# Performance work log

Hardware: AMD Instinct MI355X
Metric: run time of the kernel (lower is better)

Reference implementation:

```python
import jax, jax.numpy as jnp
import numpy as np

N = 50000
E = 800000
D = 64
EPS_BN = 1e-5
EPS_NORM = 1e-12


def _bn_train(x, gamma, beta):
    # BatchNorm1d in training mode: batch stats over axis 0, biased variance
    mu = jnp.mean(x, axis=0, keepdims=True)
    var = jnp.mean((x - mu) ** 2, axis=0, keepdims=True)
    return (x - mu) / jnp.sqrt(var + EPS_BN) * gamma + beta


def setup_inputs() -> dict:
    key = jax.random.key(0)
    ks = jax.random.split(key, 16)
    s = 1.0 / np.sqrt(D)
    s2 = 1.0 / np.sqrt(2 * D)
    return {
        "h": jax.random.normal(ks[0], (N, D), jnp.float32),
        "e": jax.random.normal(ks[1], (E, D), jnp.float32),
        "src": jax.random.randint(ks[2], (E,), 0, N, jnp.int32),
        "dst": jax.random.randint(ks[3], (E,), 0, N, jnp.int32),
        "A_W": jax.random.uniform(ks[4], (D, D), jnp.float32, -s, s),
        "A_b": jax.random.uniform(ks[5], (D,), jnp.float32, -s, s),
        "B_W": jax.random.uniform(ks[6], (D, D), jnp.float32, -s, s),
        "B_b": jax.random.uniform(ks[7], (D,), jnp.float32, -s, s),
        "C_W": jax.random.uniform(ks[8], (D, D), jnp.float32, -s, s),
        "C_b": jax.random.uniform(ks[9], (D,), jnp.float32, -s, s),
        "W_apply": jax.random.uniform(ks[10], (2 * D, D), jnp.float32, -s2, s2),
        "b_apply": jax.random.uniform(ks[11], (D,), jnp.float32, -s2, s2),
        "gamma_h": jnp.ones((D,), jnp.float32),
        "beta_h": jnp.zeros((D,), jnp.float32),
        "gamma_e": jnp.ones((D,), jnp.float32),
        "beta_e": jnp.zeros((D,), jnp.float32),
    }


def reference(h, e, src, dst, A_W, A_b, B_W, B_b, C_W, C_b,
              W_apply, b_apply, gamma_h, beta_h, gamma_e, beta_e):
    h_in, e_in = h, e
    # dropout p=0 -> identity
    Ah = h @ A_W + A_b            # [N, D]
    Bh = h @ B_W + B_b            # [N, D]
    Ce = e @ C_W + C_b            # [E, D]

    # message: e_ij = Ce + Bh_src + Bh_dst ; gated message sigma(e_ij)*Ah_src
    e_ij = Ce + Bh[src] + Bh[dst]                 # [E, D]
    msg = jax.nn.relu(jax.nn.sigmoid(e_ij) * Ah[src])  # [E, D]

    # reduce: per-destination-node max over mailbox
    c = jax.ops.segment_max(msg, dst, num_segments=N)  # [N, D], -inf if empty
    deg = jax.ops.segment_sum(jnp.ones((E,), msg.dtype), dst, num_segments=N)
    c = jnp.where(deg[:, None] > 0, c, 0.0)

    # apply/update: concat -> linear -> L2 normalize -> activation
    bundle = jnp.concatenate([h, c], axis=1) @ W_apply + b_apply  # [N, D]
    norm = jnp.sqrt(jnp.sum(bundle * bundle, axis=1, keepdims=True))
    bundle = bundle / jnp.maximum(norm, EPS_NORM)
    h_new = jax.nn.relu(bundle)

    e_new = jax.nn.relu(e_ij)

    h_new = _bn_train(h_new, gamma_h, beta_h)
    e_new = _bn_train(e_new, gamma_e, beta_e)

    h_out = h_in + h_new
    e_out = e_in + e_new
    return (h_out, e_out)
```

## Files before the change

kernel.cpp:

```cpp
#include <hip/hip_runtime.h>

typedef __attribute__((ext_vector_type(8))) short short8;
typedef __attribute__((ext_vector_type(4))) float f32x4;
typedef __attribute__((ext_vector_type(4))) unsigned int u32x4;

#define DEV static __device__ __forceinline__

constexpr int NN = 50000;
constexpr int NE = 800000;
constexpr int NT_N = NN / 16;
constexpr int NT_E = NE / 16;
constexpr int NB_SCAN = (NN + 255) / 256;
constexpr float EPS_BN = 1e-5f;
constexpr float EPS_NORM = 1e-12f;

DEV unsigned short f2b(float f) {
  unsigned u = __float_as_uint(f);
  return (unsigned short)((u + 0x7FFFu + ((u >> 16) & 1u)) >> 16);
}

DEV short8 load_a_frag(const float* __restrict__ base, int row, int kbase) {
  const f32x4* p = reinterpret_cast<const f32x4*>(base + row * 64 + kbase);
  f32x4 v0 = p[0], v1 = p[1];
  short8 a;
  a[0] = f2b(v0[0]); a[1] = f2b(v0[1]); a[2] = f2b(v0[2]); a[3] = f2b(v0[3]);
  a[4] = f2b(v1[0]); a[5] = f2b(v1[1]); a[6] = f2b(v1[2]); a[7] = f2b(v1[3]);
  return a;
}

DEV short8 load_w_frag(const float* __restrict__ W, int kbase, int c0, int lane) {
  int kr = kbase + ((lane >> 4) << 3);
  int cc = c0 + (lane & 15);
  short8 b;
#pragma unroll
  for (int j = 0; j < 8; ++j) b[j] = f2b(W[(kr + j) * 64 + cc]);
  return b;
}

DEV f32x4 mfma16(short8 a, short8 b, f32x4 c) {
  return __builtin_amdgcn_mfma_f32_16x16x32_bf16(a, b, c, 0, 0, 0);
}

__global__ void k_init(u32x4* __restrict__ cbuf4, int* __restrict__ deg,
                       float* __restrict__ stats) {
  int i = blockIdx.x * 256 + threadIdx.x;
  u32x4 z = {0u, 0u, 0u, 0u};
  cbuf4[i] = z;
  if (i < NN) deg[i] = 0;
  if (i < 512) stats[i] = 0.0f;
}

__global__ void k_deg(const int* __restrict__ dst, int* __restrict__ deg) {
  int i = blockIdx.x * 256 + threadIdx.x;
  if (i < NE) atomicAdd(&deg[dst[i]], 1);
}

__global__ void k_scan_local(const int* __restrict__ deg, int* __restrict__ off,
                             int* __restrict__ bsum) {
  __shared__ int sh[256];
  int t = threadIdx.x;
  int i = blockIdx.x * 256 + t;
  int v = (i < NN) ? deg[i] : 0;
  sh[t] = v;
  __syncthreads();
  for (int s = 1; s < 256; s <<= 1) {
    int u = (t >= s) ? sh[t - s] : 0;
    __syncthreads();
    sh[t] += u;
    __syncthreads();
  }
  if (i < NN) off[i] = sh[t] - v;
  if (t == 255) bsum[blockIdx.x] = sh[255];
}

__global__ void k_scan_base(const int* __restrict__ bsum, int* __restrict__ bbase) {
  __shared__ int sh[256];
  int t = threadIdx.x;
  int v = (t < NB_SCAN) ? bsum[t] : 0;
  sh[t] = v;
  __syncthreads();
  for (int s = 1; s < 256; s <<= 1) {
    int u = (t >= s) ? sh[t - s] : 0;
    __syncthreads();
    sh[t] += u;
    __syncthreads();
  }
  if (t < NB_SCAN) bbase[t] = sh[t] - v;
}

__global__ void k_scan_fix(const int* __restrict__ bbase, int* __restrict__ off,
                           int* __restrict__ cursor) {
  int i = blockIdx.x * 256 + threadIdx.x;
  if (i < NN) {
    int o = off[i] + bbase[blockIdx.x];
    off[i] = o;
    cursor[i] = o;
  }
}

__global__ void k_scatter(const int* __restrict__ dst, int* __restrict__ cursor,
                          int* __restrict__ perm) {
  int i = blockIdx.x * 256 + threadIdx.x;
  if (i < NE) {
    int p = atomicAdd(&cursor[dst[i]], 1);
    perm[p] = i;
  }
}

__global__ void __launch_bounds__(256) k_node_lin(
    const float* __restrict__ h, const float* __restrict__ AW,
    const float* __restrict__ Ab, const float* __restrict__ BW,
    const float* __restrict__ Bb, float* __restrict__ Ah_p,
    float* __restrict__ Bh_p) {
  int lane = threadIdx.x & 63, warp = threadIdx.x >> 6;
  int tile = blockIdx.x * 4 + warp;
  if (tile >= NT_N) return;
  int r = lane & 15;

  short8 wa[4][2], wb[4][2];
  float ab[4], bb[4];
#pragma unroll
  for (int t = 0; t < 4; ++t) {
#pragma unroll
    for (int kk = 0; kk < 2; ++kk) {
      wa[t][kk] = load_w_frag(AW, kk * 32, t * 16, lane);
      wb[t][kk] = load_w_frag(BW, kk * 32, t * 16, lane);
    }
    ab[t] = Ab[t * 16 + r];
    bb[t] = Bb[t * 16 + r];
  }

  int row0 = tile * 16;
  int ar = row0 + r, kb = (lane >> 4) * 8;
  short8 a0 = load_a_frag(h, ar, kb);
  short8 a1 = load_a_frag(h, ar, 32 + kb);

  f32x4 zero = {0.f, 0.f, 0.f, 0.f};
  f32x4 accA[4], accB[4];
#pragma unroll
  for (int t = 0; t < 4; ++t) {
    accA[t] = mfma16(a0, wa[t][0], zero);
    accA[t] = mfma16(a1, wa[t][1], accA[t]);
    accB[t] = mfma16(a0, wb[t][0], zero);
    accB[t] = mfma16(a1, wb[t][1], accB[t]);
  }
#pragma unroll
  for (int q = 0; q < 4; ++q) {
    int row = row0 + (lane >> 4) * 4 + q;
    f32x4 va = {accA[0][q] + ab[0], accA[1][q] + ab[1], accA[2][q] + ab[2],
                accA[3][q] + ab[3]};
    f32x4 vb = {accB[0][q] + bb[0], accB[1][q] + bb[1], accB[2][q] + bb[2],
                accB[3][q] + bb[3]};
    *reinterpret_cast<f32x4*>(Ah_p + row * 64 + r * 4) = va;
    *reinterpret_cast<f32x4*>(Bh_p + row * 64 + r * 4) = vb;
  }
}

__global__ void __launch_bounds__(256) k_edge_sorted(
    const float* __restrict__ e, const int* __restrict__ src,
    const int* __restrict__ dst, const int* __restrict__ perm,
    const float* __restrict__ CW, const float* __restrict__ Cb,
    const float* __restrict__ Ah_p, const float* __restrict__ Bh_p,
    float* __restrict__ cbuf, float* __restrict__ gsum,
    float* __restrict__ gsq) {
  __shared__ float msgT[4][64 * 17];
  __shared__ float ssum[64], ssq[64];
  int lane = threadIdx.x & 63, warp = threadIdx.x >> 6;
  int r = lane & 15, hi = lane >> 4;
  float* mT = msgT[warp];

  short8 cw[4][2];
  float cb4[4];
#pragma unroll
  for (int t = 0; t < 4; ++t) {
#pragma unroll
    for (int kk = 0; kk < 2; ++kk) cw[t][kk] = load_w_frag(CW, kk * 32, t * 16, lane);
    cb4[t] = Cb[t * 16 + r];
  }

  float es[4] = {0.f, 0.f, 0.f, 0.f}, eq[4] = {0.f, 0.f, 0.f, 0.f};
  f32x4 zero = {0.f, 0.f, 0.f, 0.f};
  int stride = gridDim.x * 4;

  for (int tile = blockIdx.x * 4 + warp; tile < NT_E; tile += stride) {
    int p = perm[tile * 16 + r];
    int d = dst[p];
    int s = src[p];

    int kb = hi * 8;
    short8 a0 = load_a_frag(e, p, kb);
    short8 a1 = load_a_frag(e, p, 32 + kb);

    f32x4 acc[4];
#pragma unroll
    for (int t = 0; t < 4; ++t) {
      acc[t] = mfma16(a0, cw[t][0], zero);
      acc[t] = mfma16(a1, cw[t][1], acc[t]);
    }

#pragma unroll
    for (int q = 0; q < 4; ++q) {
      int rowidx = hi * 4 + q;
      int sq_ = __shfl(s, rowidx);
      int dq_ = __shfl(d, rowidx);
      f32x4 bs = *reinterpret_cast<const f32x4*>(Bh_p + sq_ * 64 + r * 4);
      f32x4 bd = *reinterpret_cast<const f32x4*>(Bh_p + dq_ * 64 + r * 4);
      f32x4 av = *reinterpret_cast<const f32x4*>(Ah_p + sq_ * 64 + r * 4);
#pragma unroll
      for (int t = 0; t < 4; ++t) {
        float eij = acc[t][q] + cb4[t] + bs[t] + bd[t];
        float re = (eij > 0.0f) ? eij : 0.0f;
        es[t] += re;
        eq[t] += re * re;
        float sg = __fdividef(1.0f, 1.0f + __expf(-eij));
        float m = sg * av[t];
        m = (m > 0.0f) ? m : 0.0f;
        mT[(t * 16 + r) * 17 + rowidx] = m;
      }
    }

    float cur = mT[lane * 17 + 0];
    int cur_d = __shfl(d, 0);
    int run_start = 0;
#pragma unroll
    for (int row = 1; row < 16; ++row) {
      float val = mT[lane * 17 + row];
      int dr = __shfl(d, row);
      if (dr == cur_d) {
        cur = fmaxf(cur, val);
      } else {
        if (run_start == 0)
          atomicMax((unsigned*)&cbuf[cur_d * 64 + lane], __float_as_uint(cur));
        else
          cbuf[cur_d * 64 + lane] = cur;
        cur_d = dr;
        cur = val;
        run_start = row;
      }
    }
    atomicMax((unsigned*)&cbuf[cur_d * 64 + lane], __float_as_uint(cur));
  }

  if (threadIdx.x < 64) { ssum[threadIdx.x] = 0.f; ssq[threadIdx.x] = 0.f; }
  __syncthreads();
#pragma unroll
  for (int t = 0; t < 4; ++t) {
    int col = t * 16 + r;
    atomicAdd(&ssum[col], es[t]);
    atomicAdd(&ssq[col], eq[t]);
  }
  __syncthreads();
  if (threadIdx.x < 64) {
    atomicAdd(&gsum[threadIdx.x], ssum[threadIdx.x]);
    atomicAdd(&gsq[threadIdx.x], ssq[threadIdx.x]);
  }
}

__global__ void __launch_bounds__(256) k_apply(
    const float* __restrict__ h, const float* __restrict__ cbuf_f,
    const float* __restrict__ Wap, const float* __restrict__ bap,
    float* __restrict__ stage_h, float* __restrict__ gsum,
    float* __restrict__ gsq) {
  __shared__ float ssum[64], ssq[64];
  int lane = threadIdx.x & 63, warp = threadIdx.x >> 6;
  int tile = blockIdx.x * 4 + warp;
  int r = lane & 15;

  float hs[4] = {0.f, 0.f, 0.f, 0.f}, hq[4] = {0.f, 0.f, 0.f, 0.f};

  if (tile < NT_N) {
    short8 w[4][4];
    float ba[4];
#pragma unroll
    for (int t = 0; t < 4; ++t) {
#pragma unroll
      for (int kk = 0; kk < 4; ++kk) w[t][kk] = load_w_frag(Wap, kk * 32, t * 16, lane);
      ba[t] = bap[t * 16 + r];
    }

    int row0 = tile * 16;
    int ar = row0 + r, kb = (lane >> 4) * 8;
    short8 a0 = load_a_frag(h, ar, kb);
    short8 a1 = load_a_frag(h, ar, 32 + kb);
    short8 a2 = load_a_frag(cbuf_f, ar, kb);
    short8 a3 = load_a_frag(cbuf_f, ar, 32 + kb);

    f32x4 zero = {0.f, 0.f, 0.f, 0.f};
    f32x4 acc[4];
#pragma unroll
    for (int t = 0; t < 4; ++t) {
      acc[t] = mfma16(a0, w[t][0], zero);
      acc[t] = mfma16(a1, w[t][1], acc[t]);
      acc[t] = mfma16(a2, w[t][2], acc[t]);
      acc[t] = mfma16(a3, w[t][3], acc[t]);
    }

    float v[4][4];
#pragma unroll
    for (int t = 0; t < 4; ++t)
#pragma unroll
      for (int q = 0; q < 4; ++q) v[t][q] = acc[t][q] + ba[t];

#pragma unroll
    for (int q = 0; q < 4; ++q) {
      float sq = v[0][q] * v[0][q] + v[1][q] * v[1][q] + v[2][q] * v[2][q] +
                 v[3][q] * v[3][q];
      sq += __shfl_xor(sq, 1);
      sq += __shfl_xor(sq, 2);
      sq += __shfl_xor(sq, 4);
      sq += __shfl_xor(sq, 8);
      float sc = __fdividef(1.0f, fmaxf(sqrtf(sq), EPS_NORM));
      int row = row0 + (lane >> 4) * 4 + q;
#pragma unroll
      for (int t = 0; t < 4; ++t) {
        float hn = v[t][q] * sc;
        hn = (hn > 0.0f) ? hn : 0.0f;
        stage_h[row * 64 + t * 16 + r] = hn;
        hs[t] += hn;
        hq[t] += hn * hn;
      }
    }
  }

  if (threadIdx.x < 64) { ssum[threadIdx.x] = 0.f; ssq[threadIdx.x] = 0.f; }
  __syncthreads();
#pragma unroll
  for (int t = 0; t < 4; ++t) {
    int col = t * 16 + r;
    atomicAdd(&ssum[col], hs[t]);
    atomicAdd(&ssq[col], hq[t]);
  }
  __syncthreads();
  if (threadIdx.x < 64) {
    atomicAdd(&gsum[threadIdx.x], ssum[threadIdx.x]);
    atomicAdd(&gsq[threadIdx.x], ssq[threadIdx.x]);
  }
}

__global__ void k_stats(const float* __restrict__ sum_e, const float* __restrict__ sq_e,
                        const float* __restrict__ sum_h, const float* __restrict__ sq_h,
                        const float* __restrict__ gamma_e, const float* __restrict__ beta_e,
                        const float* __restrict__ gamma_h, const float* __restrict__ beta_h,
                        float* __restrict__ se, float* __restrict__ oe,
                        float* __restrict__ sh, float* __restrict__ oh) {
  int j = threadIdx.x;
  if (j < 64) {
    float mu = sum_e[j] / (float)NE;
    float var = fmaxf(sq_e[j] / (float)NE - mu * mu, 0.0f);
    float s = gamma_e[j] / sqrtf(var + EPS_BN);
    se[j] = s;
    oe[j] = beta_e[j] - mu * s;
    mu = sum_h[j] / (float)NN;
    var = fmaxf(sq_h[j] / (float)NN - mu * mu, 0.0f);
    s = gamma_h[j] / sqrtf(var + EPS_BN);
    sh[j] = s;
    oh[j] = beta_h[j] - mu * s;
  }
}

__global__ void __launch_bounds__(256) k_fin_h(const float* __restrict__ h,
                                               const float* __restrict__ sh,
                                               const float* __restrict__ oh,
                                               float* __restrict__ outh) {
  int i = (blockIdx.x * 256 + threadIdx.x) * 4;
  if (i >= NN * 64) return;
  f32x4 x = *reinterpret_cast<const f32x4*>(outh + i);
  f32x4 hv = *reinterpret_cast<const f32x4*>(h + i);
  int c0 = i & 63;
  f32x4 rr;
#pragma unroll
  for (int j = 0; j < 4; ++j) rr[j] = hv[j] + x[j] * sh[c0 + j] + oh[c0 + j];
  *reinterpret_cast<f32x4*>(outh + i) = rr;
}

__global__ void __launch_bounds__(256) k_fin_e(
    const float* __restrict__ e, const int* __restrict__ src,
    const int* __restrict__ dst, const float* __restrict__ CW,
    const float* __restrict__ Cb, const float* __restrict__ Bh_p,
    const float* __restrict__ se, const float* __restrict__ oe,
    float* __restrict__ oute) {
  int lane = threadIdx.x & 63, warp = threadIdx.x >> 6;
  int r = lane & 15;

  short8 cw[4][2];
  float cb[4], sev[4], oev[4];
#pragma unroll
  for (int t = 0; t < 4; ++t) {
#pragma unroll
    for (int kk = 0; kk < 2; ++kk) cw[t][kk] = load_w_frag(CW, kk * 32, t * 16, lane);
    cb[t] = Cb[t * 16 + r];
    sev[t] = se[t * 16 + r];
    oev[t] = oe[t * 16 + r];
  }

  f32x4 zero = {0.f, 0.f, 0.f, 0.f};
  int stride = gridDim.x * 4;

  for (int tile = blockIdx.x * 4 + warp; tile < NT_E; tile += stride) {
    int e0 = tile * 16;
    int kb = (lane >> 4) * 8;
    short8 a0 = load_a_frag(e, e0 + r, kb);
    short8 a1 = load_a_frag(e, e0 + r, 32 + kb);

    f32x4 acc[4];
#pragma unroll
    for (int t = 0; t < 4; ++t) {
      acc[t] = mfma16(a0, cw[t][0], zero);
      acc[t] = mfma16(a1, cw[t][1], acc[t]);
    }

#pragma unroll
    for (int q = 0; q < 4; ++q) {
      int er = e0 + (lane >> 4) * 4 + q;
      int s = src[er], d = dst[er];
      f32x4 bs = *reinterpret_cast<const f32x4*>(Bh_p + s * 64 + r * 4);
      f32x4 bd = *reinterpret_cast<const f32x4*>(Bh_p + d * 64 + r * 4);
#pragma unroll
      for (int t = 0; t < 4; ++t) {
        float eij = acc[t][q] + cb[t] + bs[t] + bd[t];
        float re = (eij > 0.0f) ? eij : 0.0f;
        int col = t * 16 + r;
        oute[er * 64 + col] = e[er * 64 + col] + re * sev[t] + oev[t];
      }
    }
  }
}

extern "C" void kernel_launch(void* const* d_in, const int* in_sizes, int n_in,
                              void* d_out, int out_size, void* d_ws, size_t ws_size,
                              hipStream_t stream) {
  (void)in_sizes; (void)n_in; (void)out_size; (void)ws_size;
  const float* h   = (const float*)d_in[0];
  const float* e   = (const float*)d_in[1];
  const int*   src = (const int*)d_in[2];
  const int*   dst = (const int*)d_in[3];
  const float* AW  = (const float*)d_in[4];
  const float* Ab  = (const float*)d_in[5];
  const float* BW  = (const float*)d_in[6];
  const float* Bb  = (const float*)d_in[7];
  const float* CW  = (const float*)d_in[8];
  const float* Cb  = (const float*)d_in[9];
  const float* Wap = (const float*)d_in[10];
  const float* bap = (const float*)d_in[11];
  const float* gamma_h = (const float*)d_in[12];
  const float* beta_h  = (const float*)d_in[13];
  const float* gamma_e = (const float*)d_in[14];
  const float* beta_e  = (const float*)d_in[15];

  float* ws = (float*)d_ws;
  float* Ah_p = ws;
  float* Bh_p = ws + 3200000;
  float* cbuf = ws + 6400000;
  float* stats = ws + 9600000;
  float* sum_e = stats;
  float* sq_e  = stats + 64;
  float* sum_h = stats + 128;
  float* sq_h  = stats + 192;
  float* se    = stats + 256;
  float* oe    = stats + 320;
  float* sh    = stats + 384;
  float* oh    = stats + 448;

  int* deg    = (int*)(ws + 9600512);
  int* off    = deg + NN;
  int* bsum   = off + NN;
  int* bbase  = bsum + 256;
  int* cursor = bbase + 256;
  int* perm   = cursor + NN;

  float* outh = (float*)d_out;
  float* oute = outh + (size_t)NN * 64;

  k_init<<<3125, 256, 0, stream>>>((u32x4*)cbuf, deg, stats);
  k_deg<<<(NE + 255) / 256, 256, 0, stream>>>(dst, deg);
  k_scan_local<<<NB_SCAN, 256, 0, stream>>>(deg, off, bsum);
  k_scan_base<<<1, 256, 0, stream>>>(bsum, bbase);
  k_scan_fix<<<NB_SCAN, 256, 0, stream>>>(bbase, off, cursor);
  k_scatter<<<(NE + 255) / 256, 256, 0, stream>>>(dst, cursor, perm);

  k_node_lin<<<(NT_N + 3) / 4, 256, 0, stream>>>(h, AW, Ab, BW, Bb, Ah_p, Bh_p);
  k_edge_sorted<<<2048, 256, 0, stream>>>(e, src, dst, perm, CW, Cb, Ah_p,
                                          Bh_p, cbuf, sum_e, sq_e);
  k_apply<<<(NT_N + 3) / 4, 256, 0, stream>>>(h, cbuf, Wap, bap, outh,
                                              sum_h, sq_h);
  k_stats<<<1, 64, 0, stream>>>(sum_e, sq_e, sum_h, sq_h, gamma_e, beta_e,
                                gamma_h, beta_h, se, oe, sh, oh);
  k_fin_h<<<NN * 64 / 1024, 256, 0, stream>>>(h, sh, oh, outh);
  k_fin_e<<<2048, 256, 0, stream>>>(e, src, dst, CW, Cb, Bh_p, se, oe, oute);
}
```

Measured before the change: 447.8 us.

## Stage bf16 edge pre-activations to avoid recomputing edge GEMM in finalize

The edge kernel now writes each edge's pre-activation e_ij as bf16 into a workspace stage buffer, in original edge order. The final edge pass becomes a pure streaming elementwise kernel instead of redoing the C GEMM and the random Bh gathers. Other changes: the C weight fragments live in LDS, perm is prefetched one tile ahead, messages are held in LDS as bf16, and cbuf/stage_h reuse the output buffer in place. The cost is reduced precision (bf16) for e_ij and for the max-reduced messages, plus extra LDS traffic and a 2-byte-per-element staging write and read.

```diff
diff --git a/kernel.cpp b/kernel.cpp
--- a/kernel.cpp
+++ b/kernel.cpp
@@ -1,6 +1,7 @@
 #include <hip/hip_runtime.h>
 
 typedef __attribute__((ext_vector_type(8))) short short8;
+typedef __attribute__((ext_vector_type(8))) unsigned short ushort8;
 typedef __attribute__((ext_vector_type(4))) float f32x4;
 typedef __attribute__((ext_vector_type(4))) unsigned int u32x4;
 
@@ -18,6 +19,7 @@
   unsigned u = __float_as_uint(f);
   return (unsigned short)((u + 0x7FFFu + ((u >> 16) & 1u)) >> 16);
 }
+DEV float b2f(unsigned short s) { return __uint_as_float(((unsigned)s) << 16); }
 
 DEV short8 load_a_frag(const float* __restrict__ base, int row, int kbase) {
   const f32x4* p = reinterpret_cast<const f32x4*>(base + row * 64 + kbase);
@@ -161,31 +163,41 @@
     const int* __restrict__ dst, const int* __restrict__ perm,
     const float* __restrict__ CW, const float* __restrict__ Cb,
     const float* __restrict__ Ah_p, const float* __restrict__ Bh_p,
-    float* __restrict__ cbuf, float* __restrict__ gsum,
-    float* __restrict__ gsq) {
-  __shared__ float msgT[4][64 * 17];
+    float* __restrict__ cbuf, unsigned short* __restrict__ stage,
+    float* __restrict__ gsum, float* __restrict__ gsq) {
+  __shared__ short8 cwL[8][64];
+  __shared__ unsigned short mT[4][64][18];
+  __shared__ __align__(16) unsigned short eT[4][16][72];
   __shared__ float ssum[64], ssq[64];
   int lane = threadIdx.x & 63, warp = threadIdx.x >> 6;
   int r = lane & 15, hi = lane >> 4;
-  float* mT = msgT[warp];
-
-  short8 cw[4][2];
+
+  for (int j = threadIdx.x; j < 512; j += 256) {
+    int t = j >> 7, kk = (j >> 6) & 1, ln = j & 63;
+    cwL[t * 2 + kk][ln] = load_w_frag(CW, kk * 32, t * 16, ln);
+  }
   float cb4[4];
 #pragma unroll
-  for (int t = 0; t < 4; ++t) {
-#pragma unroll
-    for (int kk = 0; kk < 2; ++kk) cw[t][kk] = load_w_frag(CW, kk * 32, t * 16, lane);
-    cb4[t] = Cb[t * 16 + r];
-  }
+  for (int t = 0; t < 4; ++t) cb4[t] = Cb[t * 16 + r];
+  __syncthreads();
+
+  unsigned short (*mTw)[18] = mT[warp];
+  unsigned short (*eTw)[72] = eT[warp];
 
   float es[4] = {0.f, 0.f, 0.f, 0.f}, eq[4] = {0.f, 0.f, 0.f, 0.f};
   f32x4 zero = {0.f, 0.f, 0.f, 0.f};
   int stride = gridDim.x * 4;
-
-  for (int tile = blockIdx.x * 4 + warp; tile < NT_E; tile += stride) {
-    int p = perm[tile * 16 + r];
-    int d = dst[p];
-    int s = src[p];
+  int tile0 = blockIdx.x * 4 + warp;
+
+  int p = 0;
+  if (tile0 < NT_E) p = perm[tile0 * 16 + r];
+
+  for (int tile = tile0; tile < NT_E; tile += stride) {
+    int tn = tile + stride;
+    int p_next = 0, d, s;
+    if (tn < NT_E) p_next = perm[tn * 16 + r];
+    d = dst[p];
+    s = src[p];
 
     int kb = hi * 8;
     short8 a0 = load_a_frag(e, p, kb);
@@ -194,8 +206,8 @@
     f32x4 acc[4];
 #pragma unroll
     for (int t = 0; t < 4; ++t) {
-      acc[t] = mfma16(a0, cw[t][0], zero);
-      acc[t] = mfma16(a1, cw[t][1], acc[t]);
+      acc[t] = mfma16(a0, cwL[t * 2][lane], zero);
+      acc[t] = mfma16(a1, cwL[t * 2 + 1][lane], acc[t]);
     }
 
 #pragma unroll
@@ -212,33 +224,47 @@
         float re = (eij > 0.0f) ? eij : 0.0f;
         es[t] += re;
         eq[t] += re * re;
+        eTw[rowidx][t * 16 + r] = f2b(eij);
         float sg = __fdividef(1.0f, 1.0f + __expf(-eij));
         float m = sg * av[t];
         m = (m > 0.0f) ? m : 0.0f;
-        mT[(t * 16 + r) * 17 + rowidx] = m;
+        mTw[t * 16 + r][rowidx] = f2b(m);
       }
     }
-
-    float cur = mT[lane * 17 + 0];
+    __builtin_amdgcn_sched_barrier(0);
+
+#pragma unroll
+    for (int it = 0; it < 2; ++it) {
+      int row = (lane >> 3) + it * 8;
+      int seg = lane & 7;
+      int er = __shfl(p, row);
+      ushort8 v = *reinterpret_cast<const ushort8*>(&eTw[row][seg * 8]);
+      *reinterpret_cast<ushort8*>(stage + (size_t)er * 64 + seg * 8) = v;
+    }
+
+    unsigned short cur = mTw[lane][0];
     int cur_d = __shfl(d, 0);
     int run_start = 0;
 #pragma unroll
     for (int row = 1; row < 16; ++row) {
-      float val = mT[lane * 17 + row];
+      unsigned short val = mTw[lane][row];
       int dr = __shfl(d, row);
       if (dr == cur_d) {
-        cur = fmaxf(cur, val);
+        cur = (val > cur) ? val : cur;
       } else {
+        float cf = b2f(cur);
         if (run_start == 0)
-          atomicMax((unsigned*)&cbuf[cur_d * 64 + lane], __float_as_uint(cur));
+          atomicMax((unsigned*)&cbuf[cur_d * 64 + lane], __float_as_uint(cf));
         else
-          cbuf[cur_d * 64 + lane] = cur;
+          cbuf[cur_d * 64 + lane] = cf;
         cur_d = dr;
         cur = val;
         run_start = row;
       }
     }
-    atomicMax((unsigned*)&cbuf[cur_d * 64 + lane], __float_as_uint(cur));
+    atomicMax((unsigned*)&cbuf[cur_d * 64 + lane], __float_as_uint(b2f(cur)));
+
+    p = p_next;
   }
 
   if (threadIdx.x < 64) { ssum[threadIdx.x] = 0.f; ssq[threadIdx.x] = 0.f; }
@@ -257,9 +283,8 @@
 }
 
 __global__ void __launch_bounds__(256) k_apply(
-    const float* __restrict__ h, const float* __restrict__ cbuf_f,
-    const float* __restrict__ Wap, const float* __restrict__ bap,
-    float* __restrict__ stage_h, float* __restrict__ gsum,
+    const float* __restrict__ h, float* hc, const float* __restrict__ Wap,
+    const float* __restrict__ bap, float* __restrict__ gsum,
     float* __restrict__ gsq) {
   __shared__ float ssum[64], ssq[64];
   int lane = threadIdx.x & 63, warp = threadIdx.x >> 6;
@@ -282,8 +307,8 @@
     int ar = row0 + r, kb = (lane >> 4) * 8;
     short8 a0 = load_a_frag(h, ar, kb);
     short8 a1 = load_a_frag(h, ar, 32 + kb);
-    short8 a2 = load_a_frag(cbuf_f, ar, kb);
-    short8 a3 = load_a_frag(cbuf_f, ar, 32 + kb);
+    short8 a2 = load_a_frag(hc, ar, kb);
+    short8 a3 = load_a_frag(hc, ar, 32 + kb);
 
     f32x4 zero = {0.f, 0.f, 0.f, 0.f};
     f32x4 acc[4];
@@ -315,7 +340,7 @@
       for (int t = 0; t < 4; ++t) {
         float hn = v[t][q] * sc;
         hn = (hn > 0.0f) ? hn : 0.0f;
-        stage_h[row * 64 + t * 16 + r] = hn;
+        hc[row * 64 + t * 16 + r] = hn;
         hs[t] += hn;
         hq[t] += hn * hn;
       }
@@ -373,57 +398,37 @@
   *reinterpret_cast<f32x4*>(outh + i) = rr;
 }
 
-__global__ void __launch_bounds__(256) k_fin_e(
-    const float* __restrict__ e, const int* __restrict__ src,
-    const int* __restrict__ dst, const float* __restrict__ CW,
-    const float* __restrict__ Cb, const float* __restrict__ Bh_p,
+__global__ void __launch_bounds__(256) k_fin_e_stream(
+    const float* __restrict__ e, const unsigned short* __restrict__ stage,
     const float* __restrict__ se, const float* __restrict__ oe,
     float* __restrict__ oute) {
-  int lane = threadIdx.x & 63, warp = threadIdx.x >> 6;
-  int r = lane & 15;
-
-  short8 cw[4][2];
-  float cb[4], sev[4], oev[4];
-#pragma unroll
-  for (int t = 0; t < 4; ++t) {
-#pragma unroll
-    for (int kk = 0; kk < 2; ++kk) cw[t][kk] = load_w_frag(CW, kk * 32, t * 16, lane);
-    cb[t] = Cb[t * 16 + r];
-    sev[t] = se[t * 16 + r];
-    oev[t] = oe[t * 16 + r];
-  }
-
-  f32x4 zero = {0.f, 0.f, 0.f, 0.f};
-  int stride = gridDim.x * 4;
-
-  for (int tile = blockIdx.x * 4 + warp; tile < NT_E; tile += stride) {
-    int e0 = tile * 16;
-    int kb = (lane >> 4) * 8;
-    short8 a0 = load_a_frag(e, e0 + r, kb);
-    short8 a1 = load_a_frag(e, e0 + r, 32 + kb);
-
-    f32x4 acc[4];
-#pragma unroll
-    for (int t = 0; t < 4; ++t) {
-      acc[t] = mfma16(a0, cw[t][0], zero);
-      acc[t] = mfma16(a1, cw[t][1], acc[t]);
-    }
-
-#pragma unroll
-    for (int q = 0; q < 4; ++q) {
-      int er = e0 + (lane >> 4) * 4 + q;
-      int s = src[er], d = dst[er];
-      f32x4 bs = *reinterpret_cast<const f32x4*>(Bh_p + s * 64 + r * 4);
-      f32x4 bd = *reinterpret_cast<const f32x4*>(Bh_p + d * 64 + r * 4);
-#pragma unroll
-      for (int t = 0; t < 4; ++t) {
-        float eij = acc[t][q] + cb[t] + bs[t] + bd[t];
-        float re = (eij > 0.0f) ? eij : 0.0f;
-        int col = t * 16 + r;
-        oute[er * 64 + col] = e[er * 64 + col] + re * sev[t] + oev[t];
-      }
-    }
-  }
+  __shared__ float s_se[64], s_oe[64];
+  if (threadIdx.x < 64) {
+    s_se[threadIdx.x] = se[threadIdx.x];
+    s_oe[threadIdx.x] = oe[threadIdx.x];
+  }
+  __syncthreads();
+  size_t i8 = (size_t)blockIdx.x * 256 + threadIdx.x;
+  size_t i = i8 * 8;
+  ushort8 sv = *reinterpret_cast<const ushort8*>(stage + i);
+  f32x4 e0 = *reinterpret_cast<const f32x4*>(e + i);
+  f32x4 e1 = *reinterpret_cast<const f32x4*>(e + i + 4);
+  int c0 = (int)(i & 63);
+  f32x4 r0, r1;
+#pragma unroll
+  for (int j = 0; j < 4; ++j) {
+    float x = b2f(sv[j]);
+    float rx = (x > 0.0f) ? x : 0.0f;
+    r0[j] = e0[j] + rx * s_se[c0 + j] + s_oe[c0 + j];
+  }
+#pragma unroll
+  for (int j = 0; j < 4; ++j) {
+    float x = b2f(sv[4 + j]);
+    float rx = (x > 0.0f) ? x : 0.0f;
+    r1[j] = e1[j] + rx * s_se[c0 + 4 + j] + s_oe[c0 + 4 + j];
+  }
+  *reinterpret_cast<f32x4*>(oute + i) = r0;
+  *reinterpret_cast<f32x4*>(oute + i + 4) = r1;
 }
 
 extern "C" void kernel_launch(void* const* d_in, const int* in_sizes, int n_in,
@@ -448,10 +453,9 @@
   const float* beta_e  = (const float*)d_in[15];
 
   float* ws = (float*)d_ws;
-  float* Ah_p = ws;
-  float* Bh_p = ws + 3200000;
-  float* cbuf = ws + 6400000;
-  float* stats = ws + 9600000;
+  float* Ah_p  = ws;
+  float* Bh_p  = ws + 3200000;
+  float* stats = ws + 6400000;
   float* sum_e = stats;
   float* sq_e  = stats + 64;
   float* sum_h = stats + 128;
@@ -461,15 +465,17 @@
   float* sh    = stats + 384;
   float* oh    = stats + 448;
 
-  int* deg    = (int*)(ws + 9600512);
+  int* deg    = (int*)(ws + 6400512);
   int* off    = deg + NN;
   int* bsum   = off + NN;
   int* bbase  = bsum + 256;
   int* cursor = bbase + 256;
   int* perm   = cursor + NN;
+  unsigned short* stage = (unsigned short*)(ws + 7351024);
 
   float* outh = (float*)d_out;
   float* oute = outh + (size_t)NN * 64;
+  float* cbuf = outh;
 
   k_init<<<3125, 256, 0, stream>>>((u32x4*)cbuf, deg, stats);
   k_deg<<<(NE + 255) / 256, 256, 0, stream>>>(dst, deg);
@@ -480,11 +486,10 @@
 
   k_node_lin<<<(NT_N + 3) / 4, 256, 0, stream>>>(h, AW, Ab, BW, Bb, Ah_p, Bh_p);
   k_edge_sorted<<<2048, 256, 0, stream>>>(e, src, dst, perm, CW, Cb, Ah_p,
-                                          Bh_p, cbuf, sum_e, sq_e);
-  k_apply<<<(NT_N + 3) / 4, 256, 0, stream>>>(h, cbuf, Wap, bap, outh,
-                                              sum_h, sq_h);
+                                          Bh_p, cbuf, stage, sum_e, sq_e);
+  k_apply<<<(NT_N + 3) / 4, 256, 0, stream>>>(h, cbuf, Wap, bap, sum_h, sq_h);
   k_stats<<<1, 64, 0, stream>>>(sum_e, sq_e, sum_h, sq_h, gamma_e, beta_e,
                                 gamma_h, beta_h, se, oe, sh, oh);
   k_fin_h<<<NN * 64 / 1024, 256, 0, stream>>>(h, sh, oh, outh);
-  k_fin_e<<<2048, 256, 0, stream>>>(e, src, dst, CW, Cb, Bh_p, se, oe, oute);
-}
+  k_fin_e_stream<<<NE * 64 / (256 * 8), 256, 0, stream>>>(e, stage, se, oe, oute);
+}
```

Result: faster. 420.9 us (-6.0%).
